# Kernel optimization log

Measured on AMD Instinct MI355X. Metric: run time of the kernel, lower is better.

## Reference

```python
import jax, jax.numpy as jnp
import numpy as np

D_H = 2048      # d_hidden
D_E = 1408      # d_expert (per routed expert)
E = 8           # n_routed_experts
K = 2           # n_experts_per_token (top-k)
N_SHARED = 2    # n_shared_experts -> shared expert dim = D_E * N_SHARED
B, S = 1, 2048
D_S = D_E * N_SHARED


def setup_inputs() -> dict:
    key = jax.random.key(0)
    ks = jax.random.split(key, 8)
    def init(k, shape, fan_in):
        # nn.Linear default init: U(-1/sqrt(fan_in), 1/sqrt(fan_in))
        bound = 1.0 / np.sqrt(fan_in)
        return jax.random.uniform(k, shape, jnp.float32, -bound, bound)
    x = jax.random.normal(ks[0], (B, S, D_H), jnp.float32)
    gate_W = init(ks[1], (E, D_H), D_H)          # router: logits = x @ gate_W.T
    Wg_e = init(ks[2], (E, D_E, D_H), D_H)       # per-expert W_gate (out,in)
    Wu_e = init(ks[3], (E, D_E, D_H), D_H)       # per-expert W_up
    Wd_e = init(ks[4], (E, D_H, D_E), D_E)       # per-expert W_down
    Wg_s = init(ks[5], (D_S, D_H), D_H)          # shared expert W_gate
    Wu_s = init(ks[6], (D_S, D_H), D_H)
    Wd_s = init(ks[7], (D_H, D_S), D_S)
    return {"x": x, "gate_W": gate_W, "Wg_e": Wg_e, "Wu_e": Wu_e,
            "Wd_e": Wd_e, "Wg_s": Wg_s, "Wu_s": Wu_s, "Wd_s": Wd_s}


def reference(x, gate_W, Wg_e, Wu_e, Wd_e, Wg_s, Wu_s, Wd_s):
    silu = jax.nn.silu
    # shared expert: SiLU-gated MLP over all tokens
    shared = (silu(x @ Wg_s.T) * (x @ Wu_s.T)) @ Wd_s.T          # [B,S,D_H]
    # gating: softmax over experts, then top-k scores/indices
    scores = jax.nn.softmax(x @ gate_W.T, axis=-1)                # [B,S,E]
    topk_scores, topk_idx = jax.lax.top_k(scores, K)              # [B,S,K]
    # dense combine weights w[t,e] = topk score if e selected else 0
    # (equivalent to the torch argsort-dispatch + scatter_reduce sum combine)
    w = jnp.sum(jax.nn.one_hot(topk_idx, E, dtype=x.dtype) * topk_scores[..., None], axis=-2)  # [B,S,E]
    xf = x.reshape(-1, D_H)                                       # [T,D_H], T = B*S
    wf = w.reshape(-1, E)                                         # [T,E]
    # per-expert SiLU-gated MLP, batched over experts
    g = jnp.einsum('td,efd->etf', xf, Wg_e)                       # [E,T,D_E]
    u = jnp.einsum('td,efd->etf', xf, Wu_e)
    h = silu(g) * u
    oe = jnp.einsum('etf,edf->etd', h, Wd_e)                      # [E,T,D_H]
    routed = jnp.einsum('etd,te->td', oe, wf).reshape(B, S, D_H)
    return routed + shared
```

## Files before the change

### kernel.cpp

```cpp
#include <hip/hip_runtime.h>

using short8 = __attribute__((ext_vector_type(8))) short;
using f32x4  = __attribute__((ext_vector_type(4))) float;
typedef unsigned short ushort_t;
typedef unsigned int u32;

#define T_TOK 2048
#define DH 2048
#define DE 1408
#define DS 2816
#define NB_GU 800
#define DN_NB 256

#define NGEc 23068672UL
#define NGSc 5767168UL
#define PA_CVT_BLOCKS 30208
#define PB_CVT_BLOCKS 14080

__device__ __forceinline__ unsigned short f2bf(float f) {
  unsigned u = __float_as_uint(f);
  u += 0x7FFF + ((u >> 16) & 1);
  return (unsigned short)(u >> 16);
}

__device__ __forceinline__ void gl_lds16(const void* g, void* l) {
  __builtin_amdgcn_global_load_lds((const __attribute__((address_space(1))) u32*)g,
                                   (__attribute__((address_space(3))) u32*)l, 16, 0, 0);
}

__device__ __forceinline__ short8 pack_bf8(float4 a, float4 b) {
  short8 o;
  o[0] = (short)f2bf(a.x); o[1] = (short)f2bf(a.y);
  o[2] = (short)f2bf(a.z); o[3] = (short)f2bf(a.w);
  o[4] = (short)f2bf(b.x); o[5] = (short)f2bf(b.y);
  o[6] = (short)f2bf(b.z); o[7] = (short)f2bf(b.w);
  return o;
}

__global__ void phaseA_kernel(const float* __restrict__ x, const float* __restrict__ gW,
                              int* __restrict__ counts, int* __restrict__ tok_e,
                              int* __restrict__ tok_slot, float* __restrict__ tok_w,
                              const float* __restrict__ Wg_e, const float* __restrict__ Wu_e,
                              const float* __restrict__ Wg_s, const float* __restrict__ Wu_s,
                              ushort_t* wbg_e, ushort_t* wbu_e,
                              ushort_t* wbg_s, ushort_t* wbu_s, ushort_t* xb) {
  int b = blockIdx.x;
  int tid = threadIdx.x;
  if (b < 512) {
    int wid = tid >> 6, lane = tid & 63;
    int t = b * 4 + wid;
    float acc[8] = {0.f,0.f,0.f,0.f,0.f,0.f,0.f,0.f};
    const float* xt = x + (size_t)t * DH;
    for (int i = lane; i < DH; i += 64) {
      float xv = xt[i];
#pragma unroll
      for (int e = 0; e < 8; e++) acc[e] += xv * gW[e * DH + i];
    }
#pragma unroll
    for (int e = 0; e < 8; e++) {
#pragma unroll
      for (int off = 32; off > 0; off >>= 1) acc[e] += __shfl_xor(acc[e], off);
    }
    if (lane == 0) {
      float mx = acc[0];
      for (int e = 1; e < 8; e++) mx = fmaxf(mx, acc[e]);
      float p[8], se = 0.f;
      for (int e = 0; e < 8; e++) { p[e] = __expf(acc[e] - mx); se += p[e]; }
      for (int e = 0; e < 8; e++) p[e] /= se;
      int i1 = 0;
      for (int e = 1; e < 8; e++) if (p[e] > p[i1]) i1 = e;
      int i2 = (i1 == 0) ? 1 : 0;
      for (int e = 0; e < 8; e++) if (e != i1 && p[e] > p[i2]) i2 = e;
      int s1 = atomicAdd(&counts[i1], 1);
      int s2 = atomicAdd(&counts[i2], 1);
      tok_e[2 * t] = i1;     tok_e[2 * t + 1] = i2;
      tok_slot[2 * t] = s1;  tok_slot[2 * t + 1] = s2;
      tok_w[2 * t] = p[i1];  tok_w[2 * t + 1] = p[i2];
    }
    return;
  }
  size_t i = (size_t)(b - 512) * 2048 + (size_t)tid * 8;
  const float* s; ushort_t* d; size_t o;
  if      (i < NGEc)                    { s = Wg_e; d = wbg_e; o = i; }
  else if (i < 2 * NGEc)                { s = Wu_e; d = wbu_e; o = i - NGEc; }
  else if (i < 2 * NGEc + NGSc)         { s = Wg_s; d = wbg_s; o = i - 2 * NGEc; }
  else if (i < 2 * NGEc + 2 * NGSc)     { s = Wu_s; d = wbu_s; o = i - 2 * NGEc - NGSc; }
  else                                  { s = x;    d = xb;    o = i - 2 * NGEc - 2 * NGSc; }
  float4 a = *(const float4*)(s + o);
  float4 bb = *(const float4*)(s + o + 4);
  *(short8*)(d + o) = pack_bf8(a, bb);
}

__global__ void prefix_assign_kernel(const int* __restrict__ counts, int* __restrict__ ebase,
                                     int* __restrict__ gu_off, int* __restrict__ dn_off,
                                     const int* __restrict__ tok_e, int* __restrict__ tok_slot,
                                     int* __restrict__ slot2tok) {
  __shared__ int sbase[8];
  if (threadIdx.x == 0) {
    int a = 0;
    for (int e = 0; e < 8; e++) { sbase[e] = a; ebase[e] = a; a += counts[e]; }
    int g = 0, d = 0;
    for (int z = 0; z < 8; z++) {
      gu_off[z] = g; dn_off[z] = d;
      int L = (counts[z] + 127) >> 7;
      g += L * 11;
      int Ld = (counts[z] + 255) >> 8;
      d += Ld * 8;
    }
    gu_off[8] = g; g += 176;
    gu_off[9] = g; g += 176;
    gu_off[10] = g;
    dn_off[8] = d; d += 64;
    dn_off[9] = d;
  }
  __syncthreads();
  for (int idx = threadIdx.x; idx < T_TOK * 2; idx += blockDim.x) {
    int e = tok_e[idx];
    int g = sbase[e] + tok_slot[idx];
    tok_slot[idx] = g;
    slot2tok[g] = idx >> 1;
  }
}

#define GU_BK 32
#define GU_OP 8192
#define GU_BUF 24576
__global__ __launch_bounds__(256, 2) void phaseB_kernel(
    const ushort_t* __restrict__ xb, const int* __restrict__ counts,
    const int* __restrict__ ebase, const int* __restrict__ gu_off,
    const int* __restrict__ slot2tok,
    const ushort_t* __restrict__ Wbg_e, const ushort_t* __restrict__ Wbu_e,
    const ushort_t* __restrict__ Wbg_s, const ushort_t* __restrict__ Wbu_s,
    ushort_t* __restrict__ h_r, ushort_t* __restrict__ h_s,
    const float* __restrict__ Wd_e, const float* __restrict__ Wd_s,
    ushort_t* wbd_e, ushort_t* wbd_s) {
  __shared__ char smem[2 * GU_BUF];
  int tid = threadIdx.x;
  if (blockIdx.x >= NB_GU) {
    size_t i = (size_t)(blockIdx.x - NB_GU) * 2048 + (size_t)tid * 8;
    const float* s; ushort_t* d; size_t o;
    if (i < NGEc) { s = Wd_e; d = wbd_e; o = i; }
    else          { s = Wd_s; d = wbd_s; o = i - NGEc; }
    float4 a = *(const float4*)(s + o);
    float4 bb = *(const float4*)(s + o + 4);
    *(short8*)(d + o) = pack_bf8(a, bb);
    return;
  }
  int b = blockIdx.x;
  int c = (b & 7) * (NB_GU >> 3) + (b >> 3);
  int off[11];
#pragma unroll
  for (int zz = 0; zz < 11; zz++) off[zz] = gu_off[zz];
  if (c >= off[10]) return;
  int z = 0;
#pragma unroll
  for (int zz = 1; zz < 10; zz++) if (c >= off[zz]) z = zz;
  int cz = c - off[z];

  bool routed = (z < 8);
  int cnt, gbase, Lm;
  const ushort_t *Bg, *Bu;
  if (routed) {
    cnt = counts[z]; gbase = ebase[z];
    Lm = (cnt + 127) >> 7;
    Bg = Wbg_e + (size_t)z * DE * DH;
    Bu = Wbu_e + (size_t)z * DE * DH;
  } else {
    cnt = T_TOK; gbase = 0; Lm = 16;
    Bg = Wbg_s + (size_t)(z - 8) * 1408 * DH;
    Bu = Wbu_s + (size_t)(z - 8) * 1408 * DH;
  }
  int mt = cz % Lm, y = cz / Lm;
  int m0 = mt * 128, n0 = y * 128;

  int lane = tid & 63, w = tid >> 6;
  int lr = lane & 15, lk = lane >> 4;
  int wr = w >> 1, wc = w & 1;

  const ushort_t* asrc[2];
  const ushort_t* gsrc[2];
  const ushort_t* usrc[2];
  int dst[2];
#pragma unroll
  for (int j = 0; j < 2; j++) {
    int r = (w * 2 + j) * 16 + (lane >> 2);
    int lrow = m0 + r;
    int tok = routed ? ((lrow < cnt) ? slot2tok[gbase + lrow] : 0) : lrow;
    int cs = (lane & 3) ^ ((r >> 1) & 3);
    asrc[j] = xb + (size_t)tok * DH + cs * 8;
    gsrc[j] = Bg + (size_t)(n0 + r) * DH + cs * 8;
    usrc[j] = Bu + (size_t)(n0 + r) * DH + cs * 8;
    dst[j] = (w * 2 + j) * 1024;
  }

  f32x4 accg[4][4] = {};
  f32x4 accu[4][4] = {};

#define GU_STAGE(buf, k0)                                              \
  {                                                                    \
    char* bb = smem + (buf) * GU_BUF;                                  \
    _Pragma("unroll")                                                  \
    for (int j = 0; j < 2; j++) {                                      \
      gl_lds16(asrc[j] + (k0), bb + dst[j]);                           \
      gl_lds16(gsrc[j] + (k0), bb + GU_OP + dst[j]);                   \
      gl_lds16(usrc[j] + (k0), bb + 2 * GU_OP + dst[j]);               \
    }                                                                  \
  }

  GU_STAGE(0, 0);
  __syncthreads();
  int cur = 0;
  for (int kc = 0; kc < DH; kc += GU_BK) {
    if (kc + GU_BK < DH) GU_STAGE(cur ^ 1, kc + GU_BK);
    const char* bb = smem + cur * GU_BUF;
    short8 af[4], bg[4], bu[4];
#pragma unroll
    for (int m = 0; m < 4; m++) {
      int rr = wr * 64 + m * 16 + lr;
      af[m] = *(const short8*)(bb + rr * 64 + ((lk ^ ((rr >> 1) & 3)) << 4));
    }
#pragma unroll
    for (int n = 0; n < 4; n++) {
      int cc = wc * 64 + n * 16 + lr;
      bg[n] = *(const short8*)(bb + GU_OP + cc * 64 + ((lk ^ ((cc >> 1) & 3)) << 4));
      bu[n] = *(const short8*)(bb + 2 * GU_OP + cc * 64 + ((lk ^ ((cc >> 1) & 3)) << 4));
    }
#pragma unroll
    for (int m = 0; m < 4; m++) {
#pragma unroll
      for (int n = 0; n < 4; n++) {
        accg[m][n] = __builtin_amdgcn_mfma_f32_16x16x32_bf16(af[m], bg[n], accg[m][n], 0, 0, 0);
        accu[m][n] = __builtin_amdgcn_mfma_f32_16x16x32_bf16(af[m], bu[n], accu[m][n], 0, 0, 0);
      }
    }
    __syncthreads();
    cur ^= 1;
  }
#pragma unroll
  for (int m = 0; m < 4; m++) {
    int rowl = m0 + wr * 64 + m * 16 + lk * 4;
#pragma unroll
    for (int n = 0; n < 4; n++) {
      int col = n0 + wc * 64 + n * 16 + lr;
#pragma unroll
      for (int j = 0; j < 4; j++) {
        float g = accg[m][n][j], u = accu[m][n][j];
        float s = g / (1.f + __expf(-g));
        unsigned short hv = f2bf(s * u);
        if (routed) {
          if (rowl + j < cnt) h_r[(size_t)(gbase + rowl + j) * DE + col] = hv;
        } else {
          h_s[(size_t)(rowl + j) * DS + (z - 8) * 1408 + col] = hv;
        }
      }
    }
  }
}

__global__ __launch_bounds__(512, 1) void down_kernel(
    const ushort_t* __restrict__ h_r, const ushort_t* __restrict__ h_s,
    const int* __restrict__ counts, const int* __restrict__ ebase,
    const int* __restrict__ dn_off,
    const ushort_t* __restrict__ Wbd_e, const ushort_t* __restrict__ Wbd_s,
    float* __restrict__ oe, float* __restrict__ out) {
  extern __shared__ char smem[];

  int b = blockIdx.x;
  int c = (b & 7) * (DN_NB >> 3) + (b >> 3);
  int off[10];
#pragma unroll
  for (int zz = 0; zz < 10; zz++) off[zz] = dn_off[zz];
  if (c >= off[9]) return;
  int z = 0;
#pragma unroll
  for (int zz = 1; zz < 9; zz++) if (c >= off[zz]) z = zz;
  int cz = c - off[z];

  bool routed = (z < 8);
  int cnt, gbase, K, Lm;
  const ushort_t* Abase;
  const ushort_t* Bw;
  if (routed) {
    cnt = counts[z]; gbase = ebase[z];
    Lm = (cnt + 255) >> 8;
    K = DE;
    Abase = h_r + (size_t)gbase * DE;
    Bw = Wbd_e + (size_t)z * DH * DE;
  } else {
    cnt = T_TOK; gbase = 0; Lm = 8;
    K = DS;
    Abase = h_s;
    Bw = Wbd_s;
  }
  int mt = cz % Lm, y = cz / Lm;
  int m0 = mt * 256, n0 = y * 256;

  int tid = threadIdx.x;
  int lane = tid & 63, w = tid >> 6;
  int lr = lane & 15, lk = lane >> 4;
  int wm = w >> 2, wn = w & 3;

  const ushort_t* asrc[4];
  const ushort_t* bsrc[4];
  int dst4[4];
#pragma unroll
  for (int j = 0; j < 4; j++) {
    int r = (w * 4 + j) * 8 + (lane >> 3);
    int cs = (lane & 7) ^ (r & 7);
    asrc[j] = Abase + (size_t)(m0 + r) * K + cs * 8;
    bsrc[j] = Bw + (size_t)(n0 + r) * K + cs * 8;
    dst4[j] = (w * 4 + j) * 1024;
  }

  f32x4 acc[8][4] = {};

#define DN_STAGE(buf, k0)                                             \
  {                                                                   \
    char* ab = smem + (buf) * 32768;                                  \
    char* wb2 = smem + 65536 + (buf) * 32768;                         \
    _Pragma("unroll")                                                 \
    for (int j = 0; j < 4; j++) {                                     \
      gl_lds16(asrc[j] + (k0), ab + dst4[j]);                         \
      gl_lds16(bsrc[j] + (k0), wb2 + dst4[j]);                        \
    }                                                                 \
  }

  const int nt = K >> 6;
  DN_STAGE(0, 0);
  __syncthreads();
  int cur = 0;
  for (int t = 0; t < nt; t++) {
    if (t + 1 < nt) DN_STAGE(cur ^ 1, (t + 1) * 64);
    const char* ab = smem + cur * 32768;
    const char* wb2 = smem + 65536 + cur * 32768;
    short8 bf[4][2];
#pragma unroll
    for (int n = 0; n < 4; n++) {
#pragma unroll
      for (int ks = 0; ks < 2; ks++) {
        int cc = wn * 64 + n * 16 + lr;
        bf[n][ks] = *(const short8*)(wb2 + cc * 128 + ((ks * 64 + lk * 16) ^ ((cc & 7) << 4)));
      }
    }
    __builtin_amdgcn_s_setprio(1);
#pragma unroll
    for (int mh = 0; mh < 2; mh++) {
      short8 af[4][2];
#pragma unroll
      for (int m4 = 0; m4 < 4; m4++) {
#pragma unroll
        for (int ks = 0; ks < 2; ks++) {
          int rr = wm * 128 + (mh * 4 + m4) * 16 + lr;
          af[m4][ks] = *(const short8*)(ab + rr * 128 + ((ks * 64 + lk * 16) ^ ((rr & 7) << 4)));
        }
      }
#pragma unroll
      for (int m4 = 0; m4 < 4; m4++) {
#pragma unroll
        for (int n = 0; n < 4; n++) {
#pragma unroll
          for (int ks = 0; ks < 2; ks++) {
            acc[mh * 4 + m4][n] = __builtin_amdgcn_mfma_f32_16x16x32_bf16(
                af[m4][ks], bf[n][ks], acc[mh * 4 + m4][n], 0, 0, 0);
          }
        }
      }
    }
    __builtin_amdgcn_s_setprio(0);
    __syncthreads();
    cur ^= 1;
  }
#pragma unroll
  for (int m = 0; m < 8; m++) {
    int rowl = m0 + wm * 128 + m * 16 + lk * 4;
#pragma unroll
    for (int n = 0; n < 4; n++) {
      int col = n0 + wn * 64 + n * 16 + lr;
#pragma unroll
      for (int j = 0; j < 4; j++) {
        if (routed) {
          if (rowl + j < cnt) oe[(size_t)(gbase + rowl + j) * DH + col] = acc[m][n][j];
        } else {
          out[(size_t)(rowl + j) * DH + col] = acc[m][n][j];
        }
      }
    }
  }
}

__global__ void combine_kernel(const int* __restrict__ tok_gslot,
                               const float* __restrict__ tok_w,
                               const float* __restrict__ oe,
                               float* __restrict__ out) {
  int t = blockIdx.x;
  int g1 = tok_gslot[2 * t], g2 = tok_gslot[2 * t + 1];
  float w1 = tok_w[2 * t], w2 = tok_w[2 * t + 1];
  int i = threadIdx.x * 8;
  const float4* p1 = (const float4*)(oe + (size_t)g1 * DH + i);
  const float4* p2 = (const float4*)(oe + (size_t)g2 * DH + i);
  float4* po = (float4*)(out + (size_t)t * DH + i);
  float4 a0 = p1[0], a1 = p1[1];
  float4 b0 = p2[0], b1 = p2[1];
  float4 o0 = po[0], o1 = po[1];
  o0.x += w1 * a0.x + w2 * b0.x;  o0.y += w1 * a0.y + w2 * b0.y;
  o0.z += w1 * a0.z + w2 * b0.z;  o0.w += w1 * a0.w + w2 * b0.w;
  o1.x += w1 * a1.x + w2 * b1.x;  o1.y += w1 * a1.y + w2 * b1.y;
  o1.z += w1 * a1.z + w2 * b1.z;  o1.w += w1 * a1.w + w2 * b1.w;
  po[0] = o0; po[1] = o1;
}

extern "C" void kernel_launch(void* const* d_in, const int* in_sizes, int n_in,
                              void* d_out, int out_size, void* d_ws, size_t ws_size,
                              hipStream_t stream) {
  const float* x    = (const float*)d_in[0];
  const float* gW   = (const float*)d_in[1];
  const float* Wg_e = (const float*)d_in[2];
  const float* Wu_e = (const float*)d_in[3];
  const float* Wd_e = (const float*)d_in[4];
  const float* Wg_s = (const float*)d_in[5];
  const float* Wu_s = (const float*)d_in[6];
  const float* Wd_s = (const float*)d_in[7];
  float* out = (float*)d_out;

  char* ws = (char*)d_ws;
  int*   counts   = (int*)ws;
  int*   ebase    = (int*)(ws + 64);
  int*   gu_off   = (int*)(ws + 128);
  int*   dn_off   = (int*)(ws + 192);
  int*   tok_e    = (int*)(ws + 256);
  int*   tok_slot = (int*)(ws + 256 + 16384);
  float* tok_w    = (float*)(ws + 256 + 32768);
  int*   slot2tok = (int*)(ws + 256 + 49152);
  ushort_t* xb  = (ushort_t*)(ws + 131072);
  ushort_t* h_r = (ushort_t*)(ws + 131072 + (size_t)T_TOK * DH * 2);
  ushort_t* h_s = h_r + (size_t)4096 * DE;
  float*    oe  = (float*)((char*)h_s + (size_t)T_TOK * DS * 2);
  ushort_t* wb  = (ushort_t*)((char*)oe + (size_t)4096 * DH * 4);
  ushort_t* wbg_e = wb;
  ushort_t* wbu_e = wb + NGEc;
  ushort_t* wbd_e = wb + 2 * NGEc;
  ushort_t* wbg_s = wb + 3 * NGEc;
  ushort_t* wbu_s = wbg_s + NGSc;
  ushort_t* wbd_s = wbg_s + 2 * NGSc;

  hipFuncSetAttribute((const void*)down_kernel,
                      hipFuncAttributeMaxDynamicSharedMemorySize, 131072);

  hipMemsetAsync(counts, 0, 64, stream);
  phaseA_kernel<<<512 + PA_CVT_BLOCKS, 256, 0, stream>>>(
      x, gW, counts, tok_e, tok_slot, tok_w,
      Wg_e, Wu_e, Wg_s, Wu_s, wbg_e, wbu_e, wbg_s, wbu_s, xb);
  prefix_assign_kernel<<<1, 256, 0, stream>>>(counts, ebase, gu_off, dn_off,
                                              tok_e, tok_slot, slot2tok);
  phaseB_kernel<<<NB_GU + PB_CVT_BLOCKS, 256, 0, stream>>>(
      xb, counts, ebase, gu_off, slot2tok, wbg_e, wbu_e, wbg_s, wbu_s, h_r, h_s,
      Wd_e, Wd_s, wbd_e, wbd_s);
  down_kernel<<<DN_NB, 512, 131072, stream>>>(
      h_r, h_s, counts, ebase, dn_off, wbd_e, wbd_s, oe, out);
  combine_kernel<<<T_TOK, 256, 0, stream>>>(tok_slot, tok_w, oe, out);
}
```

Measured before the change: 363.0 us.

## Enlarge gate/up GEMM tiles to 256x128 with 512 threads and BK=64

The fused gate/up GEMM moves from 128x128 tiles with 256 threads and K-step 32 to 256x128 tiles with 512 threads and K-step 64. It uses 128KB of dynamic LDS with an 8-way XOR swizzle, and raises wave priority around the MFMA block. The larger tiles give more reuse of each weight load and halve the number of K iterations and barriers. In exchange there are fewer, heavier blocks (one per CU), which risks load imbalance and lower occupancy. The converter blocks for the down weights also double their per-block work.

Result: faster. 343.9 us (-5.3%).

```diff
diff --git a/kernel.cpp b/kernel.cpp
--- a/kernel.cpp
+++ b/kernel.cpp
@@ -9,13 +9,13 @@
 #define DH 2048
 #define DE 1408
 #define DS 2816
-#define NB_GU 800
+#define GU_NB 440
 #define DN_NB 256
 
 #define NGEc 23068672UL
 #define NGSc 5767168UL
 #define PA_CVT_BLOCKS 30208
-#define PB_CVT_BLOCKS 14080
+#define PB_CVT_BLOCKS 7040
 
 __device__ __forceinline__ unsigned short f2bf(float f) {
   unsigned u = __float_as_uint(f);
@@ -102,13 +102,13 @@
     int g = 0, d = 0;
     for (int z = 0; z < 8; z++) {
       gu_off[z] = g; dn_off[z] = d;
-      int L = (counts[z] + 127) >> 7;
-      g += L * 11;
+      int Lg = (counts[z] + 255) >> 8;
+      g += Lg * 11;
       int Ld = (counts[z] + 255) >> 8;
       d += Ld * 8;
     }
-    gu_off[8] = g; g += 176;
-    gu_off[9] = g; g += 176;
+    gu_off[8] = g; g += 88;
+    gu_off[9] = g; g += 88;
     gu_off[10] = g;
     dn_off[8] = d; d += 64;
     dn_off[9] = d;
@@ -122,10 +122,7 @@
   }
 }
 
-#define GU_BK 32
-#define GU_OP 8192
-#define GU_BUF 24576
-__global__ __launch_bounds__(256, 2) void phaseB_kernel(
+__global__ __launch_bounds__(512, 1) void phaseB_kernel(
     const ushort_t* __restrict__ xb, const int* __restrict__ counts,
     const int* __restrict__ ebase, const int* __restrict__ gu_off,
     const int* __restrict__ slot2tok,
@@ -134,10 +131,10 @@
     ushort_t* __restrict__ h_r, ushort_t* __restrict__ h_s,
     const float* __restrict__ Wd_e, const float* __restrict__ Wd_s,
     ushort_t* wbd_e, ushort_t* wbd_s) {
-  __shared__ char smem[2 * GU_BUF];
+  extern __shared__ char smem[];
   int tid = threadIdx.x;
-  if (blockIdx.x >= NB_GU) {
-    size_t i = (size_t)(blockIdx.x - NB_GU) * 2048 + (size_t)tid * 8;
+  if (blockIdx.x >= GU_NB) {
+    size_t i = (size_t)(blockIdx.x - GU_NB) * 4096 + (size_t)tid * 8;
     const float* s; ushort_t* d; size_t o;
     if (i < NGEc) { s = Wd_e; d = wbd_e; o = i; }
     else          { s = Wd_s; d = wbd_s; o = i - NGEc; }
@@ -147,7 +144,7 @@
     return;
   }
   int b = blockIdx.x;
-  int c = (b & 7) * (NB_GU >> 3) + (b >> 3);
+  int c = (b & 7) * (GU_NB >> 3) + (b >> 3);
   int off[11];
 #pragma unroll
   for (int zz = 0; zz < 11; zz++) off[zz] = gu_off[zz];
@@ -162,86 +159,110 @@
   const ushort_t *Bg, *Bu;
   if (routed) {
     cnt = counts[z]; gbase = ebase[z];
-    Lm = (cnt + 127) >> 7;
+    Lm = (cnt + 255) >> 8;
     Bg = Wbg_e + (size_t)z * DE * DH;
     Bu = Wbu_e + (size_t)z * DE * DH;
   } else {
-    cnt = T_TOK; gbase = 0; Lm = 16;
+    cnt = T_TOK; gbase = 0; Lm = 8;
     Bg = Wbg_s + (size_t)(z - 8) * 1408 * DH;
     Bu = Wbu_s + (size_t)(z - 8) * 1408 * DH;
   }
   int mt = cz % Lm, y = cz / Lm;
-  int m0 = mt * 128, n0 = y * 128;
+  int m0 = mt * 256, n0 = y * 128;
 
   int lane = tid & 63, w = tid >> 6;
   int lr = lane & 15, lk = lane >> 4;
-  int wr = w >> 1, wc = w & 1;
-
-  const ushort_t* asrc[2];
+  int wm = w >> 1, wn = w & 1;
+
+  const ushort_t* asrc[4];
+  int adst[4];
+#pragma unroll
+  for (int j = 0; j < 4; j++) {
+    int r = (w * 4 + j) * 8 + (lane >> 3);
+    int lrow = m0 + r;
+    int tok = routed ? ((lrow < cnt) ? slot2tok[gbase + lrow] : 0) : lrow;
+    int cs = (lane & 7) ^ (r & 7);
+    asrc[j] = xb + (size_t)tok * DH + cs * 8;
+    adst[j] = (w * 4 + j) * 1024;
+  }
   const ushort_t* gsrc[2];
   const ushort_t* usrc[2];
-  int dst[2];
+  int wdst[2];
 #pragma unroll
   for (int j = 0; j < 2; j++) {
-    int r = (w * 2 + j) * 16 + (lane >> 2);
-    int lrow = m0 + r;
-    int tok = routed ? ((lrow < cnt) ? slot2tok[gbase + lrow] : 0) : lrow;
-    int cs = (lane & 3) ^ ((r >> 1) & 3);
-    asrc[j] = xb + (size_t)tok * DH + cs * 8;
+    int r = (w * 2 + j) * 8 + (lane >> 3);
+    int cs = (lane & 7) ^ (r & 7);
     gsrc[j] = Bg + (size_t)(n0 + r) * DH + cs * 8;
     usrc[j] = Bu + (size_t)(n0 + r) * DH + cs * 8;
-    dst[j] = (w * 2 + j) * 1024;
+    wdst[j] = (w * 2 + j) * 1024;
   }
 
   f32x4 accg[4][4] = {};
   f32x4 accu[4][4] = {};
 
-#define GU_STAGE(buf, k0)                                              \
-  {                                                                    \
-    char* bb = smem + (buf) * GU_BUF;                                  \
-    _Pragma("unroll")                                                  \
-    for (int j = 0; j < 2; j++) {                                      \
-      gl_lds16(asrc[j] + (k0), bb + dst[j]);                           \
-      gl_lds16(gsrc[j] + (k0), bb + GU_OP + dst[j]);                   \
-      gl_lds16(usrc[j] + (k0), bb + 2 * GU_OP + dst[j]);               \
-    }                                                                  \
-  }
-
+#define GU_STAGE(buf, k0)                                             \
+  {                                                                   \
+    char* ab = smem + (buf) * 32768;                                  \
+    char* gb = smem + 65536 + (buf) * 16384;                          \
+    char* ub = smem + 98304 + (buf) * 16384;                          \
+    _Pragma("unroll")                                                 \
+    for (int j = 0; j < 4; j++) gl_lds16(asrc[j] + (k0), ab + adst[j]); \
+    _Pragma("unroll")                                                 \
+    for (int j = 0; j < 2; j++) {                                     \
+      gl_lds16(gsrc[j] + (k0), gb + wdst[j]);                         \
+      gl_lds16(usrc[j] + (k0), ub + wdst[j]);                         \
+    }                                                                 \
+  }
+
+  const int nt = DH >> 6;
   GU_STAGE(0, 0);
   __syncthreads();
   int cur = 0;
-  for (int kc = 0; kc < DH; kc += GU_BK) {
-    if (kc + GU_BK < DH) GU_STAGE(cur ^ 1, kc + GU_BK);
-    const char* bb = smem + cur * GU_BUF;
-    short8 af[4], bg[4], bu[4];
+  for (int t = 0; t < nt; t++) {
+    if (t + 1 < nt) GU_STAGE(cur ^ 1, (t + 1) * 64);
+    const char* ab = smem + cur * 32768;
+    const char* gb = smem + 65536 + cur * 16384;
+    const char* ub = smem + 98304 + cur * 16384;
+    short8 af[4][2], bg[4][2], bu[4][2];
 #pragma unroll
     for (int m = 0; m < 4; m++) {
-      int rr = wr * 64 + m * 16 + lr;
-      af[m] = *(const short8*)(bb + rr * 64 + ((lk ^ ((rr >> 1) & 3)) << 4));
+#pragma unroll
+      for (int ks = 0; ks < 2; ks++) {
+        int rr = wm * 64 + m * 16 + lr;
+        af[m][ks] = *(const short8*)(ab + rr * 128 + ((ks * 64 + lk * 16) ^ ((rr & 7) << 4)));
+      }
     }
 #pragma unroll
     for (int n = 0; n < 4; n++) {
-      int cc = wc * 64 + n * 16 + lr;
-      bg[n] = *(const short8*)(bb + GU_OP + cc * 64 + ((lk ^ ((cc >> 1) & 3)) << 4));
-      bu[n] = *(const short8*)(bb + 2 * GU_OP + cc * 64 + ((lk ^ ((cc >> 1) & 3)) << 4));
-    }
+#pragma unroll
+      for (int ks = 0; ks < 2; ks++) {
+        int cc = wn * 64 + n * 16 + lr;
+        bg[n][ks] = *(const short8*)(gb + cc * 128 + ((ks * 64 + lk * 16) ^ ((cc & 7) << 4)));
+        bu[n][ks] = *(const short8*)(ub + cc * 128 + ((ks * 64 + lk * 16) ^ ((cc & 7) << 4)));
+      }
+    }
+    __builtin_amdgcn_s_setprio(1);
 #pragma unroll
     for (int m = 0; m < 4; m++) {
 #pragma unroll
       for (int n = 0; n < 4; n++) {
-        accg[m][n] = __builtin_amdgcn_mfma_f32_16x16x32_bf16(af[m], bg[n], accg[m][n], 0, 0, 0);
-        accu[m][n] = __builtin_amdgcn_mfma_f32_16x16x32_bf16(af[m], bu[n], accu[m][n], 0, 0, 0);
-      }
-    }
+#pragma unroll
+        for (int ks = 0; ks < 2; ks++) {
+          accg[m][n] = __builtin_amdgcn_mfma_f32_16x16x32_bf16(af[m][ks], bg[n][ks], accg[m][n], 0, 0, 0);
+          accu[m][n] = __builtin_amdgcn_mfma_f32_16x16x32_bf16(af[m][ks], bu[n][ks], accu[m][n], 0, 0, 0);
+        }
+      }
+    }
+    __builtin_amdgcn_s_setprio(0);
     __syncthreads();
     cur ^= 1;
   }
 #pragma unroll
   for (int m = 0; m < 4; m++) {
-    int rowl = m0 + wr * 64 + m * 16 + lk * 4;
+    int rowl = m0 + wm * 64 + m * 16 + lk * 4;
 #pragma unroll
     for (int n = 0; n < 4; n++) {
-      int col = n0 + wc * 64 + n * 16 + lr;
+      int col = n0 + wn * 64 + n * 16 + lr;
 #pragma unroll
       for (int j = 0; j < 4; j++) {
         float g = accg[m][n][j], u = accu[m][n][j];
@@ -443,6 +464,8 @@
   ushort_t* wbu_s = wbg_s + NGSc;
   ushort_t* wbd_s = wbg_s + 2 * NGSc;
 
+  hipFuncSetAttribute((const void*)phaseB_kernel,
+                      hipFuncAttributeMaxDynamicSharedMemorySize, 131072);
   hipFuncSetAttribute((const void*)down_kernel,
                       hipFuncAttributeMaxDynamicSharedMemorySize, 131072);
 
@@ -452,7 +475,7 @@
       Wg_e, Wu_e, Wg_s, Wu_s, wbg_e, wbu_e, wbg_s, wbu_s, xb);
   prefix_assign_kernel<<<1, 256, 0, stream>>>(counts, ebase, gu_off, dn_off,
                                               tok_e, tok_slot, slot2tok);
-  phaseB_kernel<<<NB_GU + PB_CVT_BLOCKS, 256, 0, stream>>>(
+  phaseB_kernel<<<GU_NB + PB_CVT_BLOCKS, 512, 131072, stream>>>(
       xb, counts, ebase, gu_off, slot2tok, wbg_e, wbu_e, wbg_s, wbu_s, h_r, h_s,
       Wd_e, Wd_s, wbd_e, wbd_s);
   down_kernel<<<DN_NB, 512, 131072, stream>>>(
```
